# Kernel tuning notes

Hardware: AMD Instinct MI355X
Metric: run time of the kernel (lower is better)

## Reference

```python
import jax, jax.numpy as jnp
import numpy as np

B, S, D, H = 4, 2048, 2048, 16
DH = D // H


def setup_inputs() -> dict:
    key = jax.random.key(0)
    ks = jax.random.split(key, 11)
    std = 1.0 / np.sqrt(D)
    inp = {
        'q': jax.random.normal(ks[0], (B, S, D), jnp.float32),
        'k': jax.random.normal(ks[1], (B, S, D), jnp.float32),
        'v': jax.random.normal(ks[2], (B, S, D), jnp.float32),
        'Wq': jax.random.normal(ks[3], (D, D), jnp.float32) * std,
        'bq': jnp.zeros((D,), jnp.float32),
        'Wk': jax.random.normal(ks[4], (D, D), jnp.float32) * std,
        'bk': jnp.zeros((D,), jnp.float32),
        'Wv': jax.random.normal(ks[5], (D, D), jnp.float32) * std,
        'bv': jnp.zeros((D,), jnp.float32),
        'Wo': jax.random.normal(ks[6], (D, D), jnp.float32) * std,
        'bo': jnp.zeros((D,), jnp.float32),
        # causal mask, broadcastable over batch and heads
        'mask': jnp.tril(jnp.ones((S, S), jnp.int32))[None, None],
    }
    return inp


def reference(q, k, v, Wq, bq, Wk, bk, Wv, bv, Wo, bo, mask):
    Bc = q.shape[0]
    def heads(x, W, b):
        y = x @ W + b                      # [B,S,D]
        return y.reshape(Bc, -1, H, DH).transpose(0, 2, 1, 3)  # [B,H,S,DH]
    Q = heads(q, Wq, bq)
    K = heads(k, Wk, bk)
    V = heads(v, Wv, bv)
    scores = jnp.einsum('bhqd,bhkd->bhqk', Q, K) / np.sqrt(DH).astype(jnp.float32)
    attn = jax.nn.softmax(scores, axis=-1)
    # NOTE: faithful to source — mask applied AFTER softmax with -1e9 fill
    attn = jnp.where(mask == 0, jnp.float32(-1e9), attn)
    # dropout p=0.0 -> identity
    out = jnp.einsum('bhqk,bhkd->bhqd', attn, V)
    out = out.transpose(0, 2, 1, 3).reshape(Bc, -1, D)
    return out @ Wo + bo
```

## Files before the change

kernel.cpp:

```cpp
#include <hip/hip_runtime.h>
#include <hip/hip_bf16.h>
#include <hip/hip_fp16.h>
#include <stdint.h>


#define Bdim 4
#define Sdim 2048
#define Ddim 2048
#define Hdim 16
#define DHdim 128

typedef __attribute__((ext_vector_type(4))) float f32x4;
typedef __attribute__((ext_vector_type(8))) short s16x8;
typedef __attribute__((ext_vector_type(4))) unsigned short u16x4;
typedef unsigned short u16;

__device__ __forceinline__ u16 f2b(float f) {
  union { float f; uint32_t u; } x; x.f = f;
  uint32_t r = x.u + 0x7FFFu + ((x.u >> 16) & 1u);
  return (u16)(r >> 16);
}
__device__ __forceinline__ u16 f2b_rtz(float f) {
  union { float f; uint32_t u; } x; x.f = f;
  return (u16)(x.u >> 16);
}
__device__ __forceinline__ float b2f(u16 b) {
  union { uint32_t u; float f; } x; x.u = ((uint32_t)b) << 16;
  return x.f;
}
__device__ __forceinline__ void gl_lds16(const u16* g, u16* l) {
  __builtin_amdgcn_global_load_lds(
      (const __attribute__((address_space(1))) void*)g,
      (__attribute__((address_space(3))) void*)l, 16, 0, 0);
}

__global__ __launch_bounds__(256) void wtrans_kernel(
    const float* __restrict__ Wq, const float* __restrict__ Wk,
    const float* __restrict__ Wv, const float* __restrict__ Wo,
    u16* __restrict__ WT) {
  __shared__ float tile[64][65];
  const int z = blockIdx.z;
  const float* W = (z == 0) ? Wq : (z == 1) ? Wk : (z == 2) ? Wv : Wo;
  u16* dst = WT + (size_t)z * (size_t)Ddim * Ddim;
  const int kb = blockIdx.x * 64;
  const int nb = blockIdx.y * 64;
  const int c = threadIdx.x & 63;
  const int r4 = threadIdx.x >> 6;
#pragma unroll
  for (int i = 0; i < 16; ++i) {
    int r = r4 * 16 + i;
    tile[r][c] = W[(size_t)(kb + r) * Ddim + nb + c];
  }
  __syncthreads();
#pragma unroll
  for (int i = 0; i < 16; ++i) {
    int r = r4 * 16 + i;
    dst[(size_t)(nb + r) * Ddim + kb + c] = f2b(tile[c][r]);
  }
}

__global__ __launch_bounds__(256) void xcvt_kernel(const float* __restrict__ X,
                                                   u16* __restrict__ Xb) {
  const size_t i = ((size_t)blockIdx.x * 256 + threadIdx.x) * 8;
  const uint4 a = *(const uint4*)(X + i);
  const uint4 b = *(const uint4*)(X + i + 4);
  uint4 o;
  o.x = __builtin_amdgcn_perm(a.y, a.x, 0x07060302u);
  o.y = __builtin_amdgcn_perm(a.w, a.z, 0x07060302u);
  o.z = __builtin_amdgcn_perm(b.y, b.x, 0x07060302u);
  o.w = __builtin_amdgcn_perm(b.w, b.z, 0x07060302u);
  *(uint4*)(Xb + i) = o;
}

template <int Z>
__global__ __launch_bounds__(512, 2) void gemm256_kernel(
    const u16* __restrict__ A, const u16* __restrict__ Bm,
    const float* __restrict__ bias, void* __restrict__ OutV) {
  __shared__ u16 Asl[4][256 * 32];
  __shared__ u16 Bsl[4][256 * 32];
  const int t = threadIdx.x;
  const int lane = t & 63;
  const int w = t >> 6;
  const int wm = w >> 2, wn = w & 3;
  const int l15 = lane & 15, quad = lane >> 4;
  const int n0 = blockIdx.x * 256;
  const int m0 = blockIdx.y * 256;

  const int srow = w * 32 + (lane >> 2);
  const int scb = ((((lane & 3) << 4) ^ (((srow >> 1) & 3) << 4)) >> 1);
  const u16* gA = A + (size_t)(m0 + srow) * Ddim + scb;
  const u16* gB = Bm + (size_t)(n0 + srow) * Ddim + scb;
  u16* lA0 = &Asl[0][0] + (w * 32) * 32;
  u16* lB0 = &Bsl[0][0] + (w * 32) * 32;

  int aoff[8], boff[4];
#pragma unroll
  for (int mt = 0; mt < 8; ++mt) {
    const int r = wm * 128 + mt * 16 + l15;
    aoff[mt] = r * 64 + ((quad << 4) ^ (((r >> 1) & 3) << 4));
  }
#pragma unroll
  for (int nt = 0; nt < 4; ++nt) {
    const int r = wn * 64 + nt * 16 + l15;
    boff[nt] = r * 64 + ((quad << 4) ^ (((r >> 1) & 3) << 4));
  }
  const f32x4 zero4 = {0.f, 0.f, 0.f, 0.f};
  f32x4 acc[8][4];
#pragma unroll
  for (int i = 0; i < 8; ++i)
#pragma unroll
    for (int j = 0; j < 4; ++j) acc[i][j] = zero4;

  auto stage = [&](int kt_, int buf_) {
    const u16* pa = gA + kt_ * 32;
    const u16* pb = gB + kt_ * 32;
    u16* da = lA0 + buf_ * (256 * 32);
    u16* db = lB0 + buf_ * (256 * 32);
    gl_lds16(pa, da);
    gl_lds16(pa + (size_t)16 * Ddim, da + 16 * 32);
    gl_lds16(pb, db);
    gl_lds16(pb + (size_t)16 * Ddim, db + 16 * 32);
  };
  auto compute = [&](int buf_) {
    const char* ab = (const char*)&Asl[buf_][0];
    const char* bb = (const char*)&Bsl[buf_][0];
    s16x8 af[8], bf[4];
#pragma unroll
    for (int mt = 0; mt < 8; ++mt) af[mt] = *(const s16x8*)(ab + aoff[mt]);
#pragma unroll
    for (int nt = 0; nt < 4; ++nt) bf[nt] = *(const s16x8*)(bb + boff[nt]);
    __builtin_amdgcn_s_setprio(1);
#pragma unroll
    for (int mt = 0; mt < 8; ++mt)
#pragma unroll
      for (int nt = 0; nt < 4; ++nt)
        acc[mt][nt] = __builtin_amdgcn_mfma_f32_16x16x32_bf16(
            af[mt], bf[nt], acc[mt][nt], 0, 0, 0);
    __builtin_amdgcn_s_setprio(0);
  };

  const int NK = Ddim / 32;
  stage(0, 0);
  stage(1, 1);
  stage(2, 2);
  __builtin_amdgcn_sched_barrier(0);
  asm volatile("s_waitcnt vmcnt(8)" ::: "memory");
  __builtin_amdgcn_sched_barrier(0);
  __builtin_amdgcn_s_barrier();
  int kt = 0;
  for (; kt < NK - 3; ++kt) {
    stage(kt + 3, (kt + 3) & 3);
    compute(kt & 3);
    __builtin_amdgcn_sched_barrier(0);
    asm volatile("s_waitcnt vmcnt(8)" ::: "memory");
    __builtin_amdgcn_sched_barrier(0);
    __builtin_amdgcn_s_barrier();
  }
  compute(kt & 3);
  __builtin_amdgcn_sched_barrier(0);
  asm volatile("s_waitcnt vmcnt(4)" ::: "memory");
  __builtin_amdgcn_sched_barrier(0);
  __builtin_amdgcn_s_barrier();
  ++kt;
  compute(kt & 3);
  __builtin_amdgcn_sched_barrier(0);
  asm volatile("s_waitcnt vmcnt(0)" ::: "memory");
  __builtin_amdgcn_sched_barrier(0);
  __builtin_amdgcn_s_barrier();
  ++kt;
  compute(kt & 3);

  if (Z <= 1) {
    u16* Out = (u16*)OutV;
#pragma unroll
    for (int nt = 0; nt < 4; ++nt) {
      const int gn = n0 + wn * 64 + nt * 16 + l15;
      const float bia = bias[gn];
      const int h = gn >> 7, dh = gn & 127;
#pragma unroll
      for (int mt = 0; mt < 8; ++mt) {
#pragma unroll
        for (int r = 0; r < 4; ++r) {
          const int gm = m0 + wm * 128 + mt * 16 + quad * 4 + r;
          const int b = gm >> 11, s = gm & 2047;
          Out[((size_t)(b * Hdim + h) * Sdim + s) * DHdim + dh] =
              f2b(acc[mt][nt][r] + bia);
        }
      }
    }
  } else if (Z == 2) {
    u16* Out = (u16*)OutV;
#pragma unroll
    for (int nt = 0; nt < 4; ++nt) {
      const int gn = n0 + wn * 64 + nt * 16 + l15;
      const float bia = bias[gn];
      const int h = gn >> 7, dh = gn & 127;
#pragma unroll
      for (int mt = 0; mt < 8; ++mt) {
        const int gm = m0 + wm * 128 + mt * 16 + quad * 4;
        const int b = gm >> 11, s = gm & 2047;
        u16x4 pk;
#pragma unroll
        for (int r = 0; r < 4; ++r) pk[r] = f2b(acc[mt][nt][r] + bia);
        *(u16x4*)(Out + ((size_t)(b * Hdim + h) * DHdim + dh) * Sdim + s) = pk;
      }
    }
  } else {
    float* Out = (float*)OutV;
#pragma unroll
    for (int nt = 0; nt < 4; ++nt) {
      const int gn = n0 + wn * 64 + nt * 16 + l15;
      const float bia = bias[gn];
#pragma unroll
      for (int mt = 0; mt < 8; ++mt) {
#pragma unroll
        for (int r = 0; r < 4; ++r) {
          const int gm = m0 + wm * 128 + mt * 16 + quad * 4 + r;
          Out[(size_t)gm * Ddim + gn] = acc[mt][nt][r] + bia;
        }
      }
    }
  }
}

#define SCALE2 0.12751744f
__global__ __launch_bounds__(256, 2) void attn3_kernel(
    const u16* __restrict__ Qb, const u16* __restrict__ Kb,
    const u16* __restrict__ Vt, u16* __restrict__ Ao) {
  __shared__ u16 Ks[2][64 * 128];
  __shared__ u16 Vs[2][128 * 64];
  __shared__ u16 Ps[4][32 * 64];
  const int t = threadIdx.x;
  const int lane = t & 63;
  const int w = t >> 6;
  const int l15 = lane & 15, quad = lane >> 4;
  const int bid0 = (int)blockIdx.x + ((int)blockIdx.y << 3);
  const int nbid = (bid0 & 7) * 64 + (bid0 >> 3);
  const int bx = nbid & 7;
  const int bh = nbid >> 3;
  const u16* Kbase = Kb + (size_t)bh * Sdim * DHdim;
  const u16* Vbase = Vt + (size_t)bh * DHdim * Sdim;
  u16* Pw = &Ps[w][0];
  const f32x4 zero4 = {0.f, 0.f, 0.f, 0.f};

  const int klr = lane >> 4;
  const int kcs = (lane & 15) << 4;
  const int vlr = lane >> 3;
  const int vcs = (lane & 7) << 4;

  auto stage = [&](int kt_, int buf_) {
#pragma unroll
    for (int p = 0; p < 4; ++p) {
      const int r = (w << 4) + (p << 2) + klr;
      gl_lds16(Kbase + (((size_t)kt_ * 64 + r) << 7) +
                   ((kcs ^ ((r & 7) << 4)) >> 1),
               &Ks[buf_][(w << 11) + (p << 9)]);
    }
#pragma unroll
    for (int p = 0; p < 4; ++p) {
      const int r = (w << 5) + (p << 3) + vlr;
      gl_lds16(Vbase + (size_t)r * Sdim + kt_ * 64 +
                   ((vcs ^ ((r & 7) << 4)) >> 1),
               &Vs[buf_][(w << 11) + (p << 9)]);
    }
  };

  for (int half = 0; half < 2; ++half) {
    const int qt = half ? bx : 15 - bx;
    const int qw0 = qt * 128 + w * 32;
    const int ktd = qw0 >> 6;
    const bool lowhalf = (qw0 & 63) == 0;
    const int ntiles = qt * 2 + 2;
    const u16* Qp = Qb + ((size_t)bh * Sdim + qw0) * DHdim;
    s16x8 qf[2][4];
#pragma unroll
    for (int mt = 0; mt < 2; ++mt)
#pragma unroll
      for (int ks = 0; ks < 4; ++ks)
        qf[mt][ks] = *(const s16x8*)(Qp + (size_t)(mt * 16 + l15) * DHdim +
                                     ks * 32 + quad * 8);
    f32x4 o1[2][8];
#pragma unroll
    for (int i = 0; i < 2; ++i)
#pragma unroll
      for (int j = 0; j < 8; ++j) o1[i][j] = zero4;
    float lp[2][4];
#pragma unroll
    for (int i = 0; i < 2; ++i)
#pragma unroll
      for (int j = 0; j < 4; ++j) lp[i][j] = 0.f;

    __syncthreads();
    stage(0, 0);
    __syncthreads();
    int cur = 0;
    for (int kt = 0; kt < ntiles; ++kt) {
      if (kt + 1 < ntiles) stage(kt + 1, cur ^ 1);
      if (kt <= ktd) {
        f32x4 sc[2][4];
#pragma unroll
        for (int i = 0; i < 2; ++i)
#pragma unroll
          for (int j = 0; j < 4; ++j) sc[i][j] = zero4;
#pragma unroll
        for (int ks = 0; ks < 4; ++ks) {
          s16x8 kf[4];
#pragma unroll
          for (int nt = 0; nt < 4; ++nt) {
            const int R = nt * 16 + l15;
            kf[nt] = *(const s16x8*)((const char*)&Ks[cur][0] + (R << 8) +
                                     ((ks * 64 + (quad << 4)) ^
                                      ((R & 7) << 4)));
          }
          __builtin_amdgcn_s_setprio(1);
#pragma unroll
          for (int mt = 0; mt < 2; ++mt)
#pragma unroll
            for (int nt = 0; nt < 4; ++nt)
              sc[mt][nt] = __builtin_amdgcn_mfma_f32_16x16x32_bf16(
                  qf[mt][ks], kf[nt], sc[mt][nt], 0, 0, 0);
          __builtin_amdgcn_s_setprio(0);
        }
#pragma unroll
        for (int mt = 0; mt < 2; ++mt)
#pragma unroll
          for (int r = 0; r < 4; ++r) {
            float p0 = exp2f(sc[mt][0][r] * SCALE2);
            float p1 = exp2f(sc[mt][1][r] * SCALE2);
            float p2 = exp2f(sc[mt][2][r] * SCALE2);
            float p3 = exp2f(sc[mt][3][r] * SCALE2);
            sc[mt][0][r] = p0; sc[mt][1][r] = p1;
            sc[mt][2][r] = p2; sc[mt][3][r] = p3;
            lp[mt][r] += (p0 + p1) + (p2 + p3);
          }
        const bool diag = (kt == ktd);
        if (!diag) {
#pragma unroll
          for (int mt = 0; mt < 2; ++mt)
#pragma unroll
            for (int nt = 0; nt < 4; ++nt)
#pragma unroll
              for (int r = 0; r < 4; ++r) {
                const int row = mt * 16 + quad * 4 + r;
                *(u16*)((char*)Pw + (row << 7) +
                        ((((nt * 16 + l15) << 1)) ^ ((row & 7) << 4))) =
                    f2b_rtz(sc[mt][nt][r]);
              }
        } else {
          const int ntlo = lowhalf ? 0 : 2;
#pragma unroll
          for (int mt = 0; mt < 2; ++mt)
#pragma unroll
            for (int nt = 0; nt < 4; ++nt) {
              if (!lowhalf && nt < 2) {
#pragma unroll
                for (int r = 0; r < 4; ++r) {
                  const int row = mt * 16 + quad * 4 + r;
                  *(u16*)((char*)Pw + (row << 7) +
                          ((((nt * 16 + l15) << 1)) ^ ((row & 7) << 4))) =
                      f2b_rtz(sc[mt][nt][r]);
                }
              } else if (nt >= ntlo && nt < ntlo + 2) {
                const int kg = kt * 64 + nt * 16 + l15;
#pragma unroll
                for (int r = 0; r < 4; ++r) {
                  const int qg = qw0 + mt * 16 + quad * 4 + r;
                  const int row = mt * 16 + quad * 4 + r;
                  *(u16*)((char*)Pw + (row << 7) +
                          ((((nt * 16 + l15) << 1)) ^ ((row & 7) << 4))) =
                      (kg > qg) ? (u16)0 : f2b_rtz(sc[mt][nt][r]);
                }
              }
            }
        }
        const int k2max = (diag && lowhalf) ? 1 : 2;
#pragma unroll
        for (int k2 = 0; k2 < 2; ++k2) {
          if (k2 >= k2max) break;
          s16x8 pf[2];
#pragma unroll
          for (int mt = 0; mt < 2; ++mt) {
            const int R = mt * 16 + l15;
            pf[mt] = *(const s16x8*)((const char*)Pw + (R << 7) +
                                     ((k2 * 64 + (quad << 4)) ^
                                      ((R & 7) << 4)));
          }
          __builtin_amdgcn_s_setprio(1);
#pragma unroll
          for (int nt = 0; nt < 8; ++nt) {
            const int R = nt * 16 + l15;
            const s16x8 vf = *(const s16x8*)(
                (const char*)&Vs[cur][0] + (R << 7) +
                ((k2 * 64 + (quad << 4)) ^ ((R & 7) << 4)));
#pragma unroll
            for (int mt = 0; mt < 2; ++mt)
              o1[mt][nt] = __builtin_amdgcn_mfma_f32_16x16x32_bf16(
                  pf[mt], vf, o1[mt][nt], 0, 0, 0);
          }
          __builtin_amdgcn_s_setprio(0);
        }
      }
      __syncthreads();
      cur ^= 1;
    }
    const int b = bh >> 4, h = bh & 15;
#pragma unroll
    for (int mt = 0; mt < 2; ++mt) {
#pragma unroll
      for (int r = 0; r < 4; ++r) {
        float l = lp[mt][r];
        l += __shfl_xor(l, 1);
        l += __shfl_xor(l, 2);
        l += __shfl_xor(l, 4);
        l += __shfl_xor(l, 8);
        const float invl = 1.0f / l;
        const int sq = qw0 + mt * 16 + quad * 4 + r;
        const size_t rowb = ((size_t)b * Sdim + sq) * Ddim + h * DHdim;
#pragma unroll
        for (int nt = 0; nt < 8; ++nt)
          Ao[rowb + nt * 16 + l15] = f2b(o1[mt][nt][r] * invl);
      }
    }
  }
}

__global__ __launch_bounds__(256) void vscan_kernel(const u16* __restrict__ Vt,
                                                    u16* __restrict__ Vsuf) {
  const int t = threadIdx.x, lane = t & 63, w = t >> 6;
  const int idx = blockIdx.x * 4 + w;
  const u16* src = Vt + (size_t)idx * Sdim;
  u16* dst = Vsuf + (size_t)idx * Sdim;
  const int c0 = lane * 32;
  float v[32];
#pragma unroll
  for (int p = 0; p < 4; ++p) {
    uint4 raw = *(const uint4*)(src + c0 + p * 8);
    const u16* rp = (const u16*)&raw;
#pragma unroll
    for (int j = 0; j < 8; ++j) v[p * 8 + j] = b2f(rp[j]);
  }
  float tot = 0.f;
#pragma unroll
  for (int j = 0; j < 32; ++j) tot += v[j];
  float T = tot;
#pragma unroll
  for (int off = 1; off < 64; off <<= 1) {
    float u = __shfl_down(T, off);
    if (lane + off < 64) T += u;
  }
  float s = T - tot;
  u16 outv[32];
#pragma unroll
  for (int j = 31; j >= 0; --j) {
    outv[j] = __half_as_ushort(__float2half(s));
    s += v[j];
  }
#pragma unroll
  for (int p = 0; p < 4; ++p)
    *(uint4*)(dst + c0 + p * 8) = *(uint4*)(outv + p * 8);
}

__global__ __launch_bounds__(256) void transadd_kernel(
    const u16* __restrict__ Vsuf, u16* __restrict__ Ao) {
  __shared__ float tile[64][65];
  const int qt = blockIdx.x;
  const int dt = blockIdx.y;
  const int bh = blockIdx.z;
  const int t = threadIdx.x;
  const int r = t >> 2, c0 = (t & 3) * 16;
  const u16* sp =
      Vsuf + ((size_t)bh * 128 + dt * 64 + r) * Sdim + qt * 64 + c0;
#pragma unroll
  for (int h2 = 0; h2 < 2; ++h2) {
    uint4 raw = *(const uint4*)(sp + h2 * 8);
    const u16* rp = (const u16*)&raw;
#pragma unroll
    for (int j = 0; j < 8; ++j)
      tile[c0 + h2 * 8 + j][r] = __half2float(__ushort_as_half(rp[j]));
  }
  __syncthreads();
  const int b = bh >> 4, h = bh & 15;
  u16* ap =
      Ao + ((size_t)b * Sdim + qt * 64 + r) * Ddim + h * 128 + dt * 64 + c0;
#pragma unroll
  for (int h2 = 0; h2 < 2; ++h2) {
    uint4 raw = *(uint4*)(ap + h2 * 8);
    u16* rp = (u16*)&raw;
#pragma unroll
    for (int j = 0; j < 8; ++j) {
      float a = b2f(rp[j]) - 1e9f * tile[r][c0 + h2 * 8 + j];
      rp[j] = f2b(a);
    }
    *(uint4*)(ap + h2 * 8) = raw;
  }
}

extern "C" void kernel_launch(void* const* d_in, const int* in_sizes, int n_in,
                              void* d_out, int out_size, void* d_ws,
                              size_t ws_size, hipStream_t stream) {
  (void)in_sizes; (void)n_in; (void)out_size; (void)ws_size;
  const float* q = (const float*)d_in[0];
  const float* k = (const float*)d_in[1];
  const float* v = (const float*)d_in[2];
  const float* Wq = (const float*)d_in[3];
  const float* bq = (const float*)d_in[4];
  const float* Wk = (const float*)d_in[5];
  const float* bk = (const float*)d_in[6];
  const float* Wv = (const float*)d_in[7];
  const float* bv = (const float*)d_in[8];
  const float* Wo = (const float*)d_in[9];
  const float* bo = (const float*)d_in[10];
  float* out = (float*)d_out;
  char* ws = (char*)d_ws;
  u16* WT = (u16*)(ws);
  u16* Qb = (u16*)(ws + 33554432);
  u16* Kb = (u16*)(ws + 67108864);
  u16* Vt = (u16*)(ws + 100663296);
  u16* Xb = (u16*)(ws + 134217728);
  u16* Ao = Xb;
  u16* WoT = WT + (size_t)3 * Ddim * Ddim;
  u16* Vsuf = Qb;

  wtrans_kernel<<<dim3(32, 32, 4), dim3(256), 0, stream>>>(Wq, Wk, Wv, Wo, WT);
  const float* Xs[3] = {q, k, v};
  const float* bs[3] = {bq, bk, bv};
  for (int z = 0; z < 3; ++z) {
    xcvt_kernel<<<dim3(8192), dim3(256), 0, stream>>>(Xs[z], Xb);
    if (z < 2)
      gemm256_kernel<0><<<dim3(8, 32), dim3(512), 0, stream>>>(
          Xb, WT + (size_t)z * Ddim * Ddim, bs[z], (z == 0) ? Qb : Kb);
    else
      gemm256_kernel<2><<<dim3(8, 32), dim3(512), 0, stream>>>(
          Xb, WT + (size_t)2 * Ddim * Ddim, bs[2], Vt);
  }
  attn3_kernel<<<dim3(8, 64), dim3(256), 0, stream>>>(Qb, Kb, Vt, Ao);
  vscan_kernel<<<dim3(2048), dim3(256), 0, stream>>>(Vt, Vsuf);
  transadd_kernel<<<dim3(32, 2, 64), dim3(256), 0, stream>>>(Vsuf, Ao);
  gemm256_kernel<3><<<dim3(8, 32), dim3(512), 0, stream>>>(Ao, WoT, bo, out);
}
```

Before: 810.4 us.

## Split GEMM k-step into two ping-pong phases interleaving LDS reads, prefetch, MFMA

Each k-tile iteration of the projection GEMM is split into two half phases. Each phase loads half of the A fragments, issues half of the global-to-LDS prefetch, and runs 16 MFMAs, with barriers placed between phases. This halves the live A fragment registers and interleaves memory issue with matrix math, in the style of a ping-pong schedule across waves. The cost is twice as many workgroup barriers per k-step, and the extra synchronisation could stall waves if their phases do not line up.

```diff
diff --git a/kernel.cpp b/kernel.cpp
--- a/kernel.cpp
+++ b/kernel.cpp
@@ -111,64 +111,91 @@
 #pragma unroll
     for (int j = 0; j < 4; ++j) acc[i][j] = zero4;
 
-  auto stage = [&](int kt_, int buf_) {
-    const u16* pa = gA + kt_ * 32;
-    const u16* pb = gB + kt_ * 32;
-    u16* da = lA0 + buf_ * (256 * 32);
-    u16* db = lB0 + buf_ * (256 * 32);
-    gl_lds16(pa, da);
-    gl_lds16(pa + (size_t)16 * Ddim, da + 16 * 32);
-    gl_lds16(pb, db);
-    gl_lds16(pb + (size_t)16 * Ddim, db + 16 * 32);
+  auto stage_h = [&](int kt_, int buf_, int half_) {
+    const size_t ro = (size_t)(half_ * 16) * Ddim;
+    gl_lds16(gA + kt_ * 32 + ro, lA0 + buf_ * (256 * 32) + half_ * (16 * 32));
+    gl_lds16(gB + kt_ * 32 + ro, lB0 + buf_ * (256 * 32) + half_ * (16 * 32));
   };
-  auto compute = [&](int buf_) {
+
+  s16x8 af[4], bf[4];
+  auto phase0 = [&](int buf_, bool pf_, int ktpf_) {
     const char* ab = (const char*)&Asl[buf_][0];
     const char* bb = (const char*)&Bsl[buf_][0];
-    s16x8 af[8], bf[4];
-#pragma unroll
-    for (int mt = 0; mt < 8; ++mt) af[mt] = *(const s16x8*)(ab + aoff[mt]);
+#pragma unroll
+    for (int mt = 0; mt < 4; ++mt) af[mt] = *(const s16x8*)(ab + aoff[mt]);
 #pragma unroll
     for (int nt = 0; nt < 4; ++nt) bf[nt] = *(const s16x8*)(bb + boff[nt]);
+    if (pf_) stage_h(ktpf_, ktpf_ & 3, 0);
+    __builtin_amdgcn_sched_barrier(0);
+    __builtin_amdgcn_s_barrier();
+    asm volatile("s_waitcnt lgkmcnt(0)" ::: "memory");
+    __builtin_amdgcn_sched_barrier(0);
     __builtin_amdgcn_s_setprio(1);
 #pragma unroll
-    for (int mt = 0; mt < 8; ++mt)
+    for (int mt = 0; mt < 4; ++mt)
 #pragma unroll
       for (int nt = 0; nt < 4; ++nt)
         acc[mt][nt] = __builtin_amdgcn_mfma_f32_16x16x32_bf16(
             af[mt], bf[nt], acc[mt][nt], 0, 0, 0);
     __builtin_amdgcn_s_setprio(0);
+    __builtin_amdgcn_sched_barrier(0);
+    __builtin_amdgcn_s_barrier();
   };
+  auto phase1body = [&](int buf_, bool pf_, int ktpf_) {
+    const char* ab = (const char*)&Asl[buf_][0];
+#pragma unroll
+    for (int mt = 0; mt < 4; ++mt) af[mt] = *(const s16x8*)(ab + aoff[4 + mt]);
+    if (pf_) stage_h(ktpf_, ktpf_ & 3, 1);
+    __builtin_amdgcn_sched_barrier(0);
+  };
+  auto phase1tail = [&](int buf_) {
+    __builtin_amdgcn_s_barrier();
+    asm volatile("s_waitcnt lgkmcnt(0)" ::: "memory");
+    __builtin_amdgcn_sched_barrier(0);
+    __builtin_amdgcn_s_setprio(1);
+#pragma unroll
+    for (int mt = 0; mt < 4; ++mt)
+#pragma unroll
+      for (int nt = 0; nt < 4; ++nt)
+        acc[4 + mt][nt] = __builtin_amdgcn_mfma_f32_16x16x32_bf16(
+            af[mt], bf[nt], acc[4 + mt][nt], 0, 0, 0);
+    __builtin_amdgcn_s_setprio(0);
+    __builtin_amdgcn_sched_barrier(0);
+    __builtin_amdgcn_s_barrier();
+  };
 
   const int NK = Ddim / 32;
-  stage(0, 0);
-  stage(1, 1);
-  stage(2, 2);
+  stage_h(0, 0, 0); stage_h(0, 0, 1);
+  stage_h(1, 1, 0); stage_h(1, 1, 1);
+  stage_h(2, 2, 0); stage_h(2, 2, 1);
   __builtin_amdgcn_sched_barrier(0);
   asm volatile("s_waitcnt vmcnt(8)" ::: "memory");
   __builtin_amdgcn_sched_barrier(0);
   __builtin_amdgcn_s_barrier();
   int kt = 0;
   for (; kt < NK - 3; ++kt) {
-    stage(kt + 3, (kt + 3) & 3);
-    compute(kt & 3);
-    __builtin_amdgcn_sched_barrier(0);
+    const int buf = kt & 3;
+    phase0(buf, true, kt + 3);
+    phase1body(buf, true, kt + 3);
     asm volatile("s_waitcnt vmcnt(8)" ::: "memory");
     __builtin_amdgcn_sched_barrier(0);
-    __builtin_amdgcn_s_barrier();
-  }
-  compute(kt & 3);
-  __builtin_amdgcn_sched_barrier(0);
+    phase1tail(buf);
+  }
+  phase0(kt & 3, false, 0);
+  phase1body(kt & 3, false, 0);
   asm volatile("s_waitcnt vmcnt(4)" ::: "memory");
   __builtin_amdgcn_sched_barrier(0);
-  __builtin_amdgcn_s_barrier();
+  phase1tail(kt & 3);
   ++kt;
-  compute(kt & 3);
-  __builtin_amdgcn_sched_barrier(0);
+  phase0(kt & 3, false, 0);
+  phase1body(kt & 3, false, 0);
   asm volatile("s_waitcnt vmcnt(0)" ::: "memory");
   __builtin_amdgcn_sched_barrier(0);
-  __builtin_amdgcn_s_barrier();
+  phase1tail(kt & 3);
   ++kt;
-  compute(kt & 3);
+  phase0(kt & 3, false, 0);
+  phase1body(kt & 3, false, 0);
+  phase1tail(kt & 3);
 
   if (Z <= 1) {
     u16* Out = (u16*)OutV;
```

New measurement: 751.2 us. -7.3%, faster.
